# Optimization experiments

Hardware: AMD Instinct MI355X
Metric: run time of the kernel (lower is better)

The kernel has to match this reference:

```python
import jax, jax.numpy as jnp
import numpy as np

N = 13627        # n_nodes (from negative_sampling call in source)
E_EDGES = 504378 # n_edges
F_IN = 64
H1, H2, LIN_H = 300, 100, 100  # CONFIG HIDDEN_1/HIDDEN_2/LINEAR_HIDDEN


def setup_inputs() -> dict:
    key = jax.random.key(0)
    ks = jax.random.split(key, 10)
    x = jax.random.normal(ks[0], (N, F_IN), jnp.float32)
    edge_index = jax.random.randint(ks[1], (2, E_EDGES), 0, N, dtype=jnp.int64)
    neg_edge_index = jax.random.randint(ks[2], (2, E_EDGES), 0, N, dtype=jnp.int64)
    def w(k, shape):
        return jax.random.normal(k, shape, jnp.float32) * 0.05
    return dict(
        x=x, edge_index=edge_index, neg_edge_index=neg_edge_index,
        W1=w(ks[3], (2, F_IN, H1)), b1=jnp.zeros((H1,), jnp.float32),
        W2=w(ks[4], (2, H1, H2)), b2=jnp.zeros((H2,), jnp.float32),
        W3=w(ks[5], (2, H2, 1)), b3=jnp.zeros((1,), jnp.float32),
        linW1=w(ks[6], (F_IN, LIN_H)), linb1=jnp.zeros((LIN_H,), jnp.float32),
        linW2=w(ks[7], (F_IN, LIN_H)), linb2=jnp.zeros((LIN_H,), jnp.float32),
        c1=jnp.array([0.5], jnp.float32), c2=jnp.array([0.5], jnp.float32),
    )


def _cheb_norm(edge_index, n):
    # PyG ChebConv sym normalization with lambda_max=2: Lhat = L - I,
    # off-diagonal entries -deg[src]^-1/2 * deg[dst]^-1/2, diagonal 0.
    src, dst = edge_index[0], edge_index[1]
    deg = jax.ops.segment_sum(jnp.ones(src.shape, jnp.float32), src, num_segments=n)
    dinv = jnp.where(deg > 0, jax.lax.rsqrt(jnp.maximum(deg, 1.0)), 0.0)
    return -dinv[src] * dinv[dst]


def _cheb_conv(x, W, b, src, dst, norm, n):
    # K=2: out = Tx0 @ W[0] + Tx1 @ W[1] + b, with Tx1 = Lhat @ x (gather-scale-scatter)
    tx1 = jax.ops.segment_sum(norm[:, None] * x[src], dst, num_segments=n)
    return x @ W[0] + tx1 @ W[1] + b


def reference(x, edge_index, neg_edge_index, W1, b1, W2, b2, W3, b3,
              linW1, linb1, linW2, linb2, c1, c2):
    n = x.shape[0]
    src, dst = edge_index[0], edge_index[1]
    norm = _cheb_norm(edge_index, n)
    h = jax.nn.relu(_cheb_conv(x, W1, b1, src, dst, norm, n))
    x1 = jax.nn.relu(_cheb_conv(h, W2, b2, src, dst, norm, n))
    xo = x1 + jax.nn.relu(x @ linW1 + linb1)
    z = x1 + jax.nn.relu(x @ linW2 + linb2)
    pos = jax.nn.sigmoid(jnp.sum(z[edge_index[0]] * z[edge_index[1]], axis=1))
    pos_loss = -jnp.mean(jnp.log(pos + 1e-15))
    neg = jax.nn.sigmoid(jnp.sum(z[neg_edge_index[0]] * z[neg_edge_index[1]], axis=1))
    neg_loss = -jnp.mean(jnp.log(1.0 - neg + 1e-15))
    r_loss = pos_loss + neg_loss
    out = _cheb_conv(xo, W3, b3, src, dst, norm, n)
    return out, r_loss, c1, c2
```

## Files before the change

kernel.cpp:

```cpp
#include <hip/hip_runtime.h>
#include <math.h>


typedef unsigned short ushort_t;
typedef float v2f __attribute__((ext_vector_type(2)));
typedef short bf16x8 __attribute__((ext_vector_type(8)));
typedef float f32x4 __attribute__((ext_vector_type(4)));

#define GBM 64
#define GBN 64
#define GBK 32
#define LDK 72
#define HB  256
#define PACKN 6816

__device__ inline short f2bf(float f) {
    unsigned u = __float_as_uint(f);
    u += 0x7fff + ((u >> 16) & 1);
    return (short)(u >> 16);
}
__device__ inline float bflo(unsigned w) { return __uint_as_float(w << 16); }
__device__ inline float bfhi(unsigned w) { return __uint_as_float(w & 0xffff0000u); }

__device__ inline float dot16fp8(uint4 ra, uint4 rb) {
    float dot = 0.0f;
    v2f fa, fb;
    fa = __builtin_amdgcn_cvt_pk_f32_fp8(ra.x, false);
    fb = __builtin_amdgcn_cvt_pk_f32_fp8(rb.x, false);
    dot += fa.x * fb.x + fa.y * fb.y;
    fa = __builtin_amdgcn_cvt_pk_f32_fp8(ra.x, true);
    fb = __builtin_amdgcn_cvt_pk_f32_fp8(rb.x, true);
    dot += fa.x * fb.x + fa.y * fb.y;
    fa = __builtin_amdgcn_cvt_pk_f32_fp8(ra.y, false);
    fb = __builtin_amdgcn_cvt_pk_f32_fp8(rb.y, false);
    dot += fa.x * fb.x + fa.y * fb.y;
    fa = __builtin_amdgcn_cvt_pk_f32_fp8(ra.y, true);
    fb = __builtin_amdgcn_cvt_pk_f32_fp8(rb.y, true);
    dot += fa.x * fb.x + fa.y * fb.y;
    fa = __builtin_amdgcn_cvt_pk_f32_fp8(ra.z, false);
    fb = __builtin_amdgcn_cvt_pk_f32_fp8(rb.z, false);
    dot += fa.x * fb.x + fa.y * fb.y;
    fa = __builtin_amdgcn_cvt_pk_f32_fp8(ra.z, true);
    fb = __builtin_amdgcn_cvt_pk_f32_fp8(rb.z, true);
    dot += fa.x * fb.x + fa.y * fb.y;
    fa = __builtin_amdgcn_cvt_pk_f32_fp8(ra.w, false);
    fb = __builtin_amdgcn_cvt_pk_f32_fp8(rb.w, false);
    dot += fa.x * fb.x + fa.y * fb.y;
    fa = __builtin_amdgcn_cvt_pk_f32_fp8(ra.w, true);
    fb = __builtin_amdgcn_cvt_pk_f32_fp8(rb.w, true);
    dot += fa.x * fb.x + fa.y * fb.y;
    return dot;
}

__device__ inline float loss_term(float d, int y) {
    float sg = __builtin_amdgcn_rcpf(1.0f + __expf(-d));
    return y ? __logf(1.0f - sg + 1e-15f) : __logf(sg + 1e-15f);
}

__global__ __launch_bounds__(512) void hist_both_x_kernel(
    const int* __restrict__ ei, const float* __restrict__ x,
    int* __restrict__ degp, int* __restrict__ cntp,
    ushort_t* __restrict__ xb, int Nn, int E) {
    __shared__ int lhs[PACKN];
    __shared__ int lhd[PACKN];
    for (int i = threadIdx.x; i < PACKN; i += 512) { lhs[i] = 0; lhd[i] = 0; }
    __syncthreads();
    const int b = blockIdx.x;
    const int chunk = (E + HB - 1) / HB;
    const int e0 = b * chunk;
    const int e1 = (e0 + chunk < E) ? (e0 + chunk) : E;
    for (int e = e0 + threadIdx.x; e < e1; e += 512) {
        int s = ei[e], d = ei[E + e];
        atomicAdd(&lhs[s >> 1], 1 << ((s & 1) << 4));
        atomicAdd(&lhd[d >> 1], 1 << ((d & 1) << 4));
    }
    __syncthreads();
    int* ds = degp + (size_t)b * PACKN;
    int* cs = cntp + (size_t)b * PACKN;
    for (int i = threadIdx.x; i < PACKN; i += 512) { ds[i] = lhs[i]; cs[i] = lhd[i]; }
    const int rpb = (Nn + HB - 1) / HB;
    const int r0 = b * rpb;
    const int r1 = (r0 + rpb < Nn) ? (r0 + rpb) : Nn;
    for (int i = r0 * 64 + (int)threadIdx.x; i < r1 * 64; i += 512)
        xb[i] = (ushort_t)f2bf(x[i]);
}

__global__ void merge_kernel(const int* __restrict__ degp, const int* __restrict__ cntp,
                             ushort_t* __restrict__ off, int Nal,
                             float* __restrict__ dinv, int* __restrict__ rowptr,
                             float* __restrict__ acc, int n) {
    int tid = blockIdx.x * blockDim.x + threadIdx.x;
    if (tid == 0) {
        rowptr[0] = 0;
        acc[0] = 0.0f; acc[1] = 0.0f; acc[2] = 0.0f; acc[3] = 0.0f;
    }
    int v = tid >> 2, qq = tid & 3;
    if (v >= n) return;
    const int vh = v >> 1, sh = (v & 1) << 4;
    const int b0 = qq * (HB / 4), b1 = b0 + HB / 4;
    int dsum = 0, csum = 0;
    for (int b = b0; b < b1; ++b) {
        dsum += (degp[(size_t)b * PACKN + vh] >> sh) & 0xffff;
        csum += (cntp[(size_t)b * PACKN + vh] >> sh) & 0xffff;
    }
    int dtot = dsum;
    dtot += __shfl_xor(dtot, 1, 64);
    dtot += __shfl_xor(dtot, 2, 64);
    int inc = csum;
    int t = __shfl_up(inc, 1, 64); if (qq >= 1) inc += t;
    t = __shfl_up(inc, 2, 64);     if (qq >= 2) inc += t;
    int ex = inc - csum;
    if (qq == 0) dinv[v] = (dtot > 0) ? (1.0f / sqrtf((float)dtot)) : 0.0f;
    if (qq == 3) rowptr[v + 1] = inc;
    int run = ex;
    for (int b = b0; b < b1; ++b) {
        off[(size_t)b * Nal + v] = (ushort_t)run;
        run += (cntp[(size_t)b * PACKN + vh] >> sh) & 0xffff;
    }
}

__global__ void scan_kernel(int* __restrict__ rowptr, int n) {
    __shared__ int wsum[16];
    __shared__ int carry_s;
    if (threadIdx.x == 0) carry_s = 0;
    __syncthreads();
    int nchunk = (n + 1023) / 1024;
    int wid = threadIdx.x >> 6, lane = threadIdx.x & 63;
    for (int c = 0; c < nchunk; ++c) {
        int i = c * 1024 + threadIdx.x;
        int v = (i < n) ? rowptr[i + 1] : 0;
        int s = v;
        for (int off = 1; off < 64; off <<= 1) {
            int t = __shfl_up(s, off, 64);
            if (lane >= off) s += t;
        }
        if (lane == 63) wsum[wid] = s;
        __syncthreads();
        if (wid == 0 && lane < 16) {
            int wsv = wsum[lane];
            for (int off = 1; off < 16; off <<= 1) {
                int t = __shfl_up(wsv, off, 64);
                if (lane >= off) wsv += t;
            }
            wsum[lane] = wsv;
        }
        __syncthreads();
        int base = carry_s + (wid > 0 ? wsum[wid - 1] : 0);
        int inc = base + s;
        if (i < n) rowptr[i + 1] = inc;
        __syncthreads();
        if (threadIdx.x == 1023) carry_s = inc;
        __syncthreads();
    }
}

__global__ __launch_bounds__(512) void fill_lds_kernel(
    const int* __restrict__ ei, const float* __restrict__ dinv,
    const int* __restrict__ rowptr, const ushort_t* __restrict__ off, int Nal,
    int* __restrict__ colidx, float* __restrict__ wnorm, int E) {
    __shared__ int lh[PACKN];
    for (int i = threadIdx.x; i < PACKN; i += 512) lh[i] = 0;
    __syncthreads();
    const int b = blockIdx.x;
    const int chunk = (E + HB - 1) / HB;
    const int e0 = b * chunk;
    const int e1 = (e0 + chunk < E) ? (e0 + chunk) : E;
    const ushort_t* boff = off + (size_t)b * Nal;
    for (int e = e0 + threadIdx.x; e < e1; e += 512) {
        int s = ei[e], d = ei[E + e];
        int sh = (d & 1) << 4;
        int old = atomicAdd(&lh[d >> 1], 1 << sh);
        int rank = (old >> sh) & 0xffff;
        int slot = rowptr[d] + (int)boff[d] + rank;
        colidx[slot] = s;
        wnorm[slot] = -dinv[s] * dinv[d];
    }
}

__global__ void xt_kernel(const ushort_t* __restrict__ xb, const int* __restrict__ rowptr,
                          const int* __restrict__ colidx, const float* __restrict__ wnorm,
                          ushort_t* __restrict__ XTb, int n) {
    int node = (blockIdx.x * blockDim.x + threadIdx.x) >> 6;
    if (node >= n) return;
    int lane = threadIdx.x & 63;
    int grp = lane >> 4;
    int l = lane & 15;
    int j0 = rowptr[node], j1 = rowptr[node + 1];
    float a0 = 0, a1 = 0, a2 = 0, a3 = 0;
    int j = j0 + grp;
    if (j < j1) {
        float w = wnorm[j];
        int c = colidx[j];
        uint2 r = ((const uint2*)(xb + (size_t)c * 64))[l];
        for (;;) {
            int jn = j + 4;
            bool more = jn < j1;
            float wn = 0.0f;
            uint2 rn = r;
            if (more) {
                int cn = colidx[jn];
                wn = wnorm[jn];
                rn = ((const uint2*)(xb + (size_t)cn * 64))[l];
            }
            a0 += w * bflo(r.x); a1 += w * bfhi(r.x);
            a2 += w * bflo(r.y); a3 += w * bfhi(r.y);
            if (!more) break;
            j = jn; w = wn; r = rn;
        }
    }
    a0 += __shfl_xor(a0, 16, 64); a0 += __shfl_xor(a0, 32, 64);
    a1 += __shfl_xor(a1, 16, 64); a1 += __shfl_xor(a1, 32, 64);
    a2 += __shfl_xor(a2, 16, 64); a2 += __shfl_xor(a2, 32, 64);
    a3 += __shfl_xor(a3, 16, 64); a3 += __shfl_xor(a3, 32, 64);
    if (grp == 0) {
        uint2 xv = ((const uint2*)(xb + (size_t)node * 64))[l];
        *(uint2*)&XTb[(size_t)node * 128 + l * 4] = xv;
        uint2 p;
        p.x = (unsigned)(unsigned short)f2bf(a0) | ((unsigned)(unsigned short)f2bf(a1) << 16);
        p.y = (unsigned)(unsigned short)f2bf(a2) | ((unsigned)(unsigned short)f2bf(a3) << 16);
        *(uint2*)&XTb[(size_t)node * 128 + 64 + l * 4] = p;
    }
}

__global__ __launch_bounds__(256) void gemm_mfma(
    const float* __restrict__ A, const ushort_t* __restrict__ Abf, int lda,
    const float* __restrict__ B0, const float* __restrict__ B1,
    const float* __restrict__ bias0, const float* __restrict__ bias1,
    float* __restrict__ C, int ldc, ushort_t* __restrict__ Cbf, int ldcbf,
    int cbf_mode, int Nrows, int K, int Ncols, int split, int relu) {
    __shared__ short As[GBM * LDK];
    __shared__ short Bs[GBN * LDK];
    const int bm = blockIdx.y * GBM, bn = blockIdx.x * GBN;
    const int tid = threadIdx.x;
    const int w = tid >> 6, l = tid & 63;
    const int wm = (w >> 1) * 32, wn = (w & 1) * 32;
    const int lr = l & 15;
    const int kg = l >> 4;
    const int arow = tid >> 2, aseg = tid & 3;
    const int bcol = tid & 63, bk2 = (tid >> 6) * 2;
    const int ldb0 = split, ldb1 = Ncols - split;

    const int arowg = bm + arow;
    const int bcolg = bn + bcol;
    const float* Bsrc = (bcolg < split) ? (B0 + bcolg)
                       : ((bcolg < Ncols) ? (B1 + (bcolg - split)) : nullptr);
    const int ldb = (bcolg < split) ? ldb0 : ldb1;

    f32x4 acc00 = {0,0,0,0}, acc01 = {0,0,0,0}, acc10 = {0,0,0,0}, acc11 = {0,0,0,0};

    for (int k0 = 0; k0 < K; k0 += GBK) {
        {
            int kk = k0 + aseg * 8;
            bf16x8 v;
            if (Abf) {
                if (arowg < Nrows && kk + 7 < K) {
                    v = *(const bf16x8*)&Abf[(size_t)arowg * lda + kk];
                } else {
#pragma unroll
                    for (int i = 0; i < 8; ++i)
                        v[i] = (arowg < Nrows && kk + i < K)
                             ? (short)Abf[(size_t)arowg * lda + kk + i] : (short)0;
                }
            } else if (arowg < Nrows && kk + 7 < K) {
                float4 f0 = *(const float4*)&A[(size_t)arowg * lda + kk];
                float4 f1 = *(const float4*)&A[(size_t)arowg * lda + kk + 4];
                v[0] = f2bf(f0.x); v[1] = f2bf(f0.y); v[2] = f2bf(f0.z); v[3] = f2bf(f0.w);
                v[4] = f2bf(f1.x); v[5] = f2bf(f1.y); v[6] = f2bf(f1.z); v[7] = f2bf(f1.w);
            } else {
#pragma unroll
                for (int i = 0; i < 8; ++i)
                    v[i] = (arowg < Nrows && kk + i < K)
                         ? f2bf(A[(size_t)arowg * lda + kk + i]) : (short)0;
            }
            *(bf16x8*)&As[arow * LDK + aseg * 8] = v;
        }
#pragma unroll
        for (int q = 0; q < 4; ++q) {
            int k = q * 8 + bk2;
            unsigned pw = 0u;
            if (Bsrc) {
                float f0 = (k0 + k < K) ? Bsrc[(size_t)(k0 + k) * ldb] : 0.0f;
                float f1 = (k0 + k + 1 < K) ? Bsrc[(size_t)(k0 + k + 1) * ldb] : 0.0f;
                pw = (unsigned)(unsigned short)f2bf(f0)
                   | ((unsigned)(unsigned short)f2bf(f1) << 16);
            }
            *(unsigned*)&Bs[bcol * LDK + k] = pw;
        }
        __syncthreads();
        bf16x8 a0 = *(const bf16x8*)&As[(wm + lr) * LDK + kg * 8];
        bf16x8 a1 = *(const bf16x8*)&As[(wm + 16 + lr) * LDK + kg * 8];
        bf16x8 b0 = *(const bf16x8*)&Bs[(wn + lr) * LDK + kg * 8];
        bf16x8 b1 = *(const bf16x8*)&Bs[(wn + 16 + lr) * LDK + kg * 8];
        acc00 = __builtin_amdgcn_mfma_f32_16x16x32_bf16(a0, b0, acc00, 0, 0, 0);
        acc01 = __builtin_amdgcn_mfma_f32_16x16x32_bf16(a0, b1, acc01, 0, 0, 0);
        acc10 = __builtin_amdgcn_mfma_f32_16x16x32_bf16(a1, b0, acc10, 0, 0, 0);
        acc11 = __builtin_amdgcn_mfma_f32_16x16x32_bf16(a1, b1, acc11, 0, 0, 0);
        __syncthreads();
    }
#pragma unroll
    for (int i = 0; i < 2; ++i) {
        int rbase = bm + wm + i * 16 + kg * 4;
#pragma unroll
        for (int j = 0; j < 2; ++j) {
            int col = bn + wn + j * 16 + lr;
            if (col >= Ncols) continue;
            float bv = (col < split) ? (bias0 ? bias0[col] : 0.0f)
                                     : (bias1 ? bias1[col - split] : 0.0f);
            f32x4 a = (i == 0) ? (j == 0 ? acc00 : acc01) : (j == 0 ? acc10 : acc11);
#pragma unroll
            for (int r = 0; r < 4; ++r) {
                int row = rbase + r;
                if (row >= Nrows) continue;
                float o = a[r] + bv;
                if (relu) o = fmaxf(o, 0.0f);
                if (cbf_mode == 2)
                    Cbf[(size_t)row * ldcbf + col] = (ushort_t)f2bf(o);
                else if (cbf_mode == 1 && col >= split)
                    Cbf[(size_t)row * 128 + (col - split)] = (ushort_t)f2bf(o);
                else
                    C[(size_t)row * ldc + col] = o;
            }
        }
    }
}

__global__ void segsum_combine1_kernel(const ushort_t* __restrict__ hb,
                                       const int* __restrict__ rowptr, const int* __restrict__ colidx,
                                       const float* __restrict__ wnorm,
                                       const float* __restrict__ G2a, const float* __restrict__ b2,
                                       float* __restrict__ x1, int n) {
    int node = (blockIdx.x * blockDim.x + threadIdx.x) >> 6;
    if (node >= n) return;
    int lane = threadIdx.x & 63;
    int grp = lane >> 4;
    int l = lane & 15;
    int j0 = rowptr[node], j1 = rowptr[node + 1];
    float acc[8] = {};
    int j = j0 + grp;
    if (j < j1) {
        float w = wnorm[j];
        int c = colidx[j];
        uint4 r = ((const uint4*)(hb + (size_t)c * 128))[l];
        for (;;) {
            int jn = j + 4;
            bool more = jn < j1;
            float wn = 0.0f;
            uint4 rn = r;
            if (more) {
                int cn = colidx[jn];
                wn = wnorm[jn];
                rn = ((const uint4*)(hb + (size_t)cn * 128))[l];
            }
            acc[0] += w * bflo(r.x); acc[1] += w * bfhi(r.x);
            acc[2] += w * bflo(r.y); acc[3] += w * bfhi(r.y);
            acc[4] += w * bflo(r.z); acc[5] += w * bfhi(r.z);
            acc[6] += w * bflo(r.w); acc[7] += w * bfhi(r.w);
            if (!more) break;
            j = jn; w = wn; r = rn;
        }
    }
#pragma unroll
    for (int k = 0; k < 8; ++k) {
        acc[k] += __shfl_xor(acc[k], 16, 64);
        acc[k] += __shfl_xor(acc[k], 32, 64);
    }
    if (grp == 0) {
        int f = l * 8;
        if (f < 100) {
            float4 g0 = *(const float4*)&G2a[(size_t)node * 100 + f];
            float4 bv0 = *(const float4*)&b2[f];
            float4 o0;
            o0.x = fmaxf(g0.x + acc[0] + bv0.x, 0.0f);
            o0.y = fmaxf(g0.y + acc[1] + bv0.y, 0.0f);
            o0.z = fmaxf(g0.z + acc[2] + bv0.z, 0.0f);
            o0.w = fmaxf(g0.w + acc[3] + bv0.w, 0.0f);
            *(float4*)&x1[(size_t)node * 100 + f] = o0;
            if (f + 8 <= 100) {
                float4 g1 = *(const float4*)&G2a[(size_t)node * 100 + f + 4];
                float4 bv1 = *(const float4*)&b2[f + 4];
                float4 o1;
                o1.x = fmaxf(g1.x + acc[4] + bv1.x, 0.0f);
                o1.y = fmaxf(g1.y + acc[5] + bv1.y, 0.0f);
                o1.z = fmaxf(g1.z + acc[6] + bv1.z, 0.0f);
                o1.w = fmaxf(g1.w + acc[7] + bv1.w, 0.0f);
                *(float4*)&x1[(size_t)node * 100 + f + 4] = o1;
            }
        }
    }
}

__global__ void combine2_kernel(const float* __restrict__ S, const float* __restrict__ x1,
                                const float* __restrict__ w3b,
                                float* __restrict__ xo, unsigned* __restrict__ zf,
                                float* __restrict__ sv, int n) {
    int idx = blockIdx.x * blockDim.x + threadIdx.x;
    if (idx >= n * 32) return;
    int i = idx >> 5, q = idx & 31;
    unsigned w = 0u;
    float part = 0.0f;
    if (q < 25) {
        float4 s1 = *(const float4*)&S[(size_t)i * 200 + q * 4];
        float4 s2 = *(const float4*)&S[(size_t)i * 200 + 100 + q * 4];
        float4 xv = *(const float4*)&x1[(size_t)i * 100 + q * 4];
        float4 a, b;
        a.x = xv.x + fmaxf(s1.x, 0.0f); a.y = xv.y + fmaxf(s1.y, 0.0f);
        a.z = xv.z + fmaxf(s1.z, 0.0f); a.w = xv.w + fmaxf(s1.w, 0.0f);
        b.x = xv.x + fmaxf(s2.x, 0.0f); b.y = xv.y + fmaxf(s2.y, 0.0f);
        b.z = xv.z + fmaxf(s2.z, 0.0f); b.w = xv.w + fmaxf(s2.w, 0.0f);
        *(float4*)&xo[(size_t)i * 100 + q * 4] = a;
        w = (unsigned)__builtin_amdgcn_cvt_pk_fp8_f32(b.x, b.y, 0, false);
        w = (unsigned)__builtin_amdgcn_cvt_pk_fp8_f32(b.z, b.w, (int)w, true);
        float4 wv = *(const float4*)&w3b[q * 4];
        part = a.x * wv.x + a.y * wv.y + a.z * wv.z + a.w * wv.w;
    }
    zf[(size_t)i * 32 + q] = w;
#pragma unroll
    for (int off = 16; off > 0; off >>= 1)
        part += __shfl_xor(part, off, 32);
    if (q == 0) sv[i] = part;
}

__global__ __launch_bounds__(256) void edge_loss_fp8_kernel(
    const unsigned* __restrict__ zf, const int* __restrict__ ei,
    const int* __restrict__ nei, int E, float* __restrict__ accv) {
    const int y = blockIdx.y;
    const int* __restrict__ lst = y ? nei : ei;
    const int l = threadIdx.x & 7;
    const int g = (blockIdx.x * blockDim.x + threadIdx.x) >> 3;
    const int ng = (gridDim.x * blockDim.x) >> 3;
    const int stride2 = 2 * ng;
    float s = 0.0f;
    const int gA = g, gB = g + ng;
    int niterA = (gA < E) ? ((E - 1 - gA) / stride2 + 1) : 0;
    int niterB = (gB < E) ? ((E - 1 - gB) / stride2 + 1) : 0;
    if (niterA > 0) {
        int eB0 = (gB < E) ? gB : (E - 1);
        int eA1 = (gA + stride2 < E) ? (gA + stride2) : (E - 1);
        int eB1 = (gB + stride2 < E) ? (gB + stride2) : (E - 1);
        int aA0 = lst[gA], bA0 = lst[E + gA];
        int aB0 = lst[eB0], bB0 = lst[E + eB0];
        int aA1 = lst[eA1], bA1 = lst[E + eA1];
        int aB1 = lst[eB1], bB1 = lst[E + eB1];
        uint4 raA = *(const uint4*)&zf[(size_t)aA0 * 32 + l * 4];
        uint4 rbA = *(const uint4*)&zf[(size_t)bA0 * 32 + l * 4];
        uint4 raB = *(const uint4*)&zf[(size_t)aB0 * 32 + l * 4];
        uint4 rbB = *(const uint4*)&zf[(size_t)bB0 * 32 + l * 4];
        for (int t = 0; t < niterA; ++t) {
            int eA2 = gA + (t + 2) * stride2; eA2 = (eA2 < E) ? eA2 : (E - 1);
            int eB2 = gB + (t + 2) * stride2; eB2 = (eB2 < E) ? eB2 : (E - 1);
            int aA2 = lst[eA2], bA2 = lst[E + eA2];
            int aB2 = lst[eB2], bB2 = lst[E + eB2];
            uint4 raA1 = *(const uint4*)&zf[(size_t)aA1 * 32 + l * 4];
            uint4 rbA1 = *(const uint4*)&zf[(size_t)bA1 * 32 + l * 4];
            uint4 raB1 = *(const uint4*)&zf[(size_t)aB1 * 32 + l * 4];
            uint4 rbB1 = *(const uint4*)&zf[(size_t)bB1 * 32 + l * 4];
            float dA = dot16fp8(raA, rbA);
            float dB = dot16fp8(raB, rbB);
            dA += __shfl_xor(dA, 1, 8); dB += __shfl_xor(dB, 1, 8);
            dA += __shfl_xor(dA, 2, 8); dB += __shfl_xor(dB, 2, 8);
            dA += __shfl_xor(dA, 4, 8); dB += __shfl_xor(dB, 4, 8);
            if (l == 0) {
                s += loss_term(dA, y);
                if (t < niterB) s += loss_term(dB, y);
            }
            aA1 = aA2; bA1 = bA2; aB1 = aB2; bB1 = bB2;
            raA = raA1; rbA = rbA1; raB = raB1; rbB = rbB1;
        }
    }
    __shared__ float red[256];
    red[threadIdx.x] = s;
    __syncthreads();
    for (int st = 128; st > 0; st >>= 1) {
        if (threadIdx.x < st) red[threadIdx.x] += red[threadIdx.x + st];
        __syncthreads();
    }
    if (threadIdx.x == 0) atomicAdd(&accv[y], red[0]);
}

__global__ void out_finalize_kernel(const float* __restrict__ xo, const float* __restrict__ W3,
                                    const float* __restrict__ b3, const int* __restrict__ rowptr,
                                    const int* __restrict__ colidx, const float* __restrict__ wnorm,
                                    const float* __restrict__ sv, const float* __restrict__ accv,
                                    const float* __restrict__ c1, const float* __restrict__ c2,
                                    float* __restrict__ out, int n, int E) {
    int i = blockIdx.x * blockDim.x + threadIdx.x;
    if (i == 0) {
        out[n]     = -(accv[0] + accv[1]) / (float)E;
        out[n + 1] = c1[0];
        out[n + 2] = c2[0];
    }
    if (i >= n) return;
    const float4* a = (const float4*)(xo + (size_t)i * 100);
    const float4* wv = (const float4*)W3;
    float acc = b3[0];
#pragma unroll
    for (int q = 0; q < 25; ++q) {
        float4 va = a[q], vw = wv[q];
        acc += va.x * vw.x + va.y * vw.y + va.z * vw.z + va.w * vw.w;
    }
    int j1 = rowptr[i + 1];
    for (int j = rowptr[i]; j < j1; ++j)
        acc += wnorm[j] * sv[colidx[j]];
    out[i] = acc;
}

extern "C" void kernel_launch(void* const* d_in, const int* in_sizes, int n_in,
                              void* d_out, int out_size, void* d_ws, size_t ws_size,
                              hipStream_t stream) {
    (void)n_in; (void)out_size; (void)ws_size;
    const float* x   = (const float*)d_in[0];
    const int*   ei  = (const int*)d_in[1];
    const int*   nei = (const int*)d_in[2];
    const float* W1  = (const float*)d_in[3];
    const float* b1  = (const float*)d_in[4];
    const float* W2  = (const float*)d_in[5];
    const float* b2  = (const float*)d_in[6];
    const float* W3  = (const float*)d_in[7];
    const float* b3  = (const float*)d_in[8];
    const float* lw1 = (const float*)d_in[9];
    const float* lb1 = (const float*)d_in[10];
    const float* lw2 = (const float*)d_in[11];
    const float* lb2 = (const float*)d_in[12];
    const float* c1  = (const float*)d_in[13];
    const float* c2  = (const float*)d_in[14];

    const int Nn = in_sizes[0] / 64;
    const int E  = in_sizes[1] / 2;

    const size_t Nal = ((size_t)Nn + 5) & ~(size_t)3;
    const size_t Eal = ((size_t)E + 3) & ~(size_t)3;
    const int LDH = 304;

    float* ws       = (float*)d_ws;
    float* acc      = ws;
    float* dinv     = acc + 4;
    int*   rowptr   = (int*)(dinv + Nal);
    int*   colidx   = rowptr + Nal;
    float* wnorm    = (float*)(colidx + Eal);
    int*   degp     = (int*)(wnorm + Eal);
    int*   cntp     = degp + (size_t)HB * PACKN;
    ushort_t* offus = (ushort_t*)(cntp + (size_t)HB * PACKN);
    ushort_t* xb    = offus + (size_t)HB * Nal;
    ushort_t* XTb   = xb + (size_t)Nn * 64;
    ushort_t* hb    = XTb + (size_t)Nn * 128;
    float* G2a      = (float*)(hb + (size_t)Nn * LDH);
    float* x1       = G2a + (size_t)Nn * 100;
    float* xo       = x1 + (size_t)Nn * 100;
    float* S        = xo + (size_t)Nn * 100;
    size_t zoff     = (size_t)(S + (size_t)Nn * 200 - ws);
    zoff = (zoff + 31) & ~(size_t)31;
    unsigned* zf    = (unsigned*)(ws + zoff);
    size_t hoff2    = zoff + (size_t)Nn * 32 + 63;
    hoff2 &= ~(size_t)63;
    ushort_t* hWb   = (ushort_t*)(ws + hoff2);
    float* sv       = ws + hoff2 + (size_t)Nn * 64;
    const int MB = (Nn + GBM - 1) / GBM;

    hist_both_x_kernel<<<HB, 512, 0, stream>>>(ei, x, degp, cntp, xb, Nn, E);
    merge_kernel<<<(4 * Nn + 255) / 256, 256, 0, stream>>>(degp, cntp, offus, (int)Nal,
                                                           dinv, rowptr, acc, Nn);
    scan_kernel<<<1, 1024, 0, stream>>>(rowptr, Nn);
    fill_lds_kernel<<<HB, 512, 0, stream>>>(ei, dinv, rowptr, offus, (int)Nal,
                                            colidx, wnorm, E);

    xt_kernel<<<(Nn + 3) / 4, 256, 0, stream>>>(xb, rowptr, colidx, wnorm, XTb, Nn);
    gemm_mfma<<<dim3(5, MB), 256, 0, stream>>>(
        nullptr, XTb, 128, W1, nullptr, b1, nullptr,
        nullptr, 0, hb, LDH, 2, Nn, 128, 300, 300, 1);

    gemm_mfma<<<dim3(4, MB), 256, 0, stream>>>(
        nullptr, hb, LDH, W2, W2 + 300 * 100, nullptr, nullptr,
        G2a, 100, hWb, 0, 1, Nn, 300, 200, 100, 0);
    segsum_combine1_kernel<<<(Nn + 3) / 4, 256, 0, stream>>>(hWb, rowptr, colidx, wnorm,
                                                             G2a, b2, x1, Nn);

    gemm_mfma<<<dim3(4, MB), 256, 0, stream>>>(
        nullptr, xb, 64, lw1, lw2, lb1, lb2,
        S, 200, nullptr, 0, 0, Nn, 64, 200, 100, 0);
    combine2_kernel<<<(Nn * 32 + 255) / 256, 256, 0, stream>>>(S, x1, W3 + 100,
                                                               xo, zf, sv, Nn);

    edge_loss_fp8_kernel<<<dim3(1024, 2), 256, 0, stream>>>(zf, ei, nei, E, acc);

    out_finalize_kernel<<<(Nn + 255) / 256, 256, 0, stream>>>(
        xo, W3, b3, rowptr, colidx, wnorm, sv, acc, c1, c2, (float*)d_out, Nn, E);
}
```

Before: 215.7 us.

## Fuse linear-branch GEMMs into first ChebConv GEMM and restructure edge-loss loop

The first MFMA GEMM now computes three column groups at once (W1 over the full 128-wide [x, Lx] input plus lin1 and lin2 over only the first 64 K columns), which removes a separate GEMM launch and a second read of x. A new output mode writes the ReLU'd bf16 hidden activations and the fp32 linear outputs to separate buffers. The edge-loss kernel drops its software-pipelined prefetch in favour of processing four independent edges per iteration, and its grid is doubled. The fused GEMM wastes some K iterations on zero-padded B for the linear columns, and the edge kernel loses cross-iteration prefetch.

```diff
diff --git a/kernel.cpp b/kernel.cpp
--- a/kernel.cpp
+++ b/kernel.cpp
@@ -223,11 +223,12 @@
 }
 
 __global__ __launch_bounds__(256) void gemm_mfma(
-    const float* __restrict__ A, const ushort_t* __restrict__ Abf, int lda,
-    const float* __restrict__ B0, const float* __restrict__ B1,
-    const float* __restrict__ bias0, const float* __restrict__ bias1,
+    const ushort_t* __restrict__ Abf, int lda,
+    const float* __restrict__ B0, const float* __restrict__ B1, const float* __restrict__ B2,
+    const float* __restrict__ bias0, const float* __restrict__ bias1, const float* __restrict__ bias2,
+    int split, int split2, int klim1,
     float* __restrict__ C, int ldc, ushort_t* __restrict__ Cbf, int ldcbf,
-    int cbf_mode, int Nrows, int K, int Ncols, int split, int relu) {
+    int cbf_mode, int Nrows, int K, int Ncols, int relu) {
     __shared__ short As[GBM * LDK];
     __shared__ short Bs[GBN * LDK];
     const int bm = blockIdx.y * GBM, bn = blockIdx.x * GBN;
@@ -238,13 +239,14 @@
     const int kg = l >> 4;
     const int arow = tid >> 2, aseg = tid & 3;
     const int bcol = tid & 63, bk2 = (tid >> 6) * 2;
-    const int ldb0 = split, ldb1 = Ncols - split;
 
     const int arowg = bm + arow;
     const int bcolg = bn + bcol;
-    const float* Bsrc = (bcolg < split) ? (B0 + bcolg)
-                       : ((bcolg < Ncols) ? (B1 + (bcolg - split)) : nullptr);
-    const int ldb = (bcolg < split) ? ldb0 : ldb1;
+    const float* Bsrc = nullptr;
+    int ldb = 1, Klim = K;
+    if (bcolg < split)                            { Bsrc = B0 + bcolg; ldb = split; Klim = K; }
+    else if (bcolg < split2 && bcolg < Ncols)     { Bsrc = B1 + (bcolg - split); ldb = split2 - split; Klim = klim1; }
+    else if (bcolg < Ncols)                       { Bsrc = B2 + (bcolg - split2); ldb = Ncols - split2; Klim = klim1; }
 
     f32x4 acc00 = {0,0,0,0}, acc01 = {0,0,0,0}, acc10 = {0,0,0,0}, acc11 = {0,0,0,0};
 
@@ -252,25 +254,13 @@
         {
             int kk = k0 + aseg * 8;
             bf16x8 v;
-            if (Abf) {
-                if (arowg < Nrows && kk + 7 < K) {
-                    v = *(const bf16x8*)&Abf[(size_t)arowg * lda + kk];
-                } else {
-#pragma unroll
-                    for (int i = 0; i < 8; ++i)
-                        v[i] = (arowg < Nrows && kk + i < K)
-                             ? (short)Abf[(size_t)arowg * lda + kk + i] : (short)0;
-                }
-            } else if (arowg < Nrows && kk + 7 < K) {
-                float4 f0 = *(const float4*)&A[(size_t)arowg * lda + kk];
-                float4 f1 = *(const float4*)&A[(size_t)arowg * lda + kk + 4];
-                v[0] = f2bf(f0.x); v[1] = f2bf(f0.y); v[2] = f2bf(f0.z); v[3] = f2bf(f0.w);
-                v[4] = f2bf(f1.x); v[5] = f2bf(f1.y); v[6] = f2bf(f1.z); v[7] = f2bf(f1.w);
+            if (arowg < Nrows && kk + 7 < K) {
+                v = *(const bf16x8*)&Abf[(size_t)arowg * lda + kk];
             } else {
 #pragma unroll
                 for (int i = 0; i < 8; ++i)
                     v[i] = (arowg < Nrows && kk + i < K)
-                         ? f2bf(A[(size_t)arowg * lda + kk + i]) : (short)0;
+                         ? (short)Abf[(size_t)arowg * lda + kk + i] : (short)0;
             }
             *(bf16x8*)&As[arow * LDK + aseg * 8] = v;
         }
@@ -279,8 +269,8 @@
             int k = q * 8 + bk2;
             unsigned pw = 0u;
             if (Bsrc) {
-                float f0 = (k0 + k < K) ? Bsrc[(size_t)(k0 + k) * ldb] : 0.0f;
-                float f1 = (k0 + k + 1 < K) ? Bsrc[(size_t)(k0 + k + 1) * ldb] : 0.0f;
+                float f0 = (k0 + k < Klim) ? Bsrc[(size_t)(k0 + k) * ldb] : 0.0f;
+                float f1 = (k0 + k + 1 < Klim) ? Bsrc[(size_t)(k0 + k + 1) * ldb] : 0.0f;
                 pw = (unsigned)(unsigned short)f2bf(f0)
                    | ((unsigned)(unsigned short)f2bf(f1) << 16);
             }
@@ -304,21 +294,30 @@
         for (int j = 0; j < 2; ++j) {
             int col = bn + wn + j * 16 + lr;
             if (col >= Ncols) continue;
-            float bv = (col < split) ? (bias0 ? bias0[col] : 0.0f)
-                                     : (bias1 ? bias1[col - split] : 0.0f);
+            float bv;
+            if (col < split)       bv = bias0 ? bias0[col] : 0.0f;
+            else if (col < split2) bv = bias1 ? bias1[col - split] : 0.0f;
+            else                   bv = bias2 ? bias2[col - split2] : 0.0f;
             f32x4 a = (i == 0) ? (j == 0 ? acc00 : acc01) : (j == 0 ? acc10 : acc11);
 #pragma unroll
             for (int r = 0; r < 4; ++r) {
                 int row = rbase + r;
                 if (row >= Nrows) continue;
                 float o = a[r] + bv;
-                if (relu) o = fmaxf(o, 0.0f);
-                if (cbf_mode == 2)
+                if (cbf_mode == 3) {
+                    if (col < split)
+                        Cbf[(size_t)row * ldcbf + col] = (ushort_t)f2bf(fmaxf(o, 0.0f));
+                    else
+                        C[(size_t)row * ldc + (col - split)] = o;
+                } else if (cbf_mode == 2) {
+                    if (relu) o = fmaxf(o, 0.0f);
                     Cbf[(size_t)row * ldcbf + col] = (ushort_t)f2bf(o);
-                else if (cbf_mode == 1 && col >= split)
+                } else if (cbf_mode == 1 && col >= split) {
                     Cbf[(size_t)row * 128 + (col - split)] = (ushort_t)f2bf(o);
-                else
+                } else {
+                    if (relu) o = fmaxf(o, 0.0f);
                     C[(size_t)row * ldc + col] = o;
+                }
             }
         }
     }
@@ -428,43 +427,39 @@
     const int l = threadIdx.x & 7;
     const int g = (blockIdx.x * blockDim.x + threadIdx.x) >> 3;
     const int ng = (gridDim.x * blockDim.x) >> 3;
-    const int stride2 = 2 * ng;
+    const int stride4 = 4 * ng;
     float s = 0.0f;
-    const int gA = g, gB = g + ng;
-    int niterA = (gA < E) ? ((E - 1 - gA) / stride2 + 1) : 0;
-    int niterB = (gB < E) ? ((E - 1 - gB) / stride2 + 1) : 0;
-    if (niterA > 0) {
-        int eB0 = (gB < E) ? gB : (E - 1);
-        int eA1 = (gA + stride2 < E) ? (gA + stride2) : (E - 1);
-        int eB1 = (gB + stride2 < E) ? (gB + stride2) : (E - 1);
-        int aA0 = lst[gA], bA0 = lst[E + gA];
-        int aB0 = lst[eB0], bB0 = lst[E + eB0];
-        int aA1 = lst[eA1], bA1 = lst[E + eA1];
-        int aB1 = lst[eB1], bB1 = lst[E + eB1];
-        uint4 raA = *(const uint4*)&zf[(size_t)aA0 * 32 + l * 4];
-        uint4 rbA = *(const uint4*)&zf[(size_t)bA0 * 32 + l * 4];
-        uint4 raB = *(const uint4*)&zf[(size_t)aB0 * 32 + l * 4];
-        uint4 rbB = *(const uint4*)&zf[(size_t)bB0 * 32 + l * 4];
-        for (int t = 0; t < niterA; ++t) {
-            int eA2 = gA + (t + 2) * stride2; eA2 = (eA2 < E) ? eA2 : (E - 1);
-            int eB2 = gB + (t + 2) * stride2; eB2 = (eB2 < E) ? eB2 : (E - 1);
-            int aA2 = lst[eA2], bA2 = lst[E + eA2];
-            int aB2 = lst[eB2], bB2 = lst[E + eB2];
-            uint4 raA1 = *(const uint4*)&zf[(size_t)aA1 * 32 + l * 4];
-            uint4 rbA1 = *(const uint4*)&zf[(size_t)bA1 * 32 + l * 4];
-            uint4 raB1 = *(const uint4*)&zf[(size_t)aB1 * 32 + l * 4];
-            uint4 rbB1 = *(const uint4*)&zf[(size_t)bB1 * 32 + l * 4];
-            float dA = dot16fp8(raA, rbA);
-            float dB = dot16fp8(raB, rbB);
-            dA += __shfl_xor(dA, 1, 8); dB += __shfl_xor(dB, 1, 8);
-            dA += __shfl_xor(dA, 2, 8); dB += __shfl_xor(dB, 2, 8);
-            dA += __shfl_xor(dA, 4, 8); dB += __shfl_xor(dB, 4, 8);
-            if (l == 0) {
-                s += loss_term(dA, y);
-                if (t < niterB) s += loss_term(dB, y);
-            }
-            aA1 = aA2; bA1 = bA2; aB1 = aB2; bB1 = bB2;
-            raA = raA1; rbA = rbA1; raB = raB1; rbB = rbB1;
+    int n0 = (g < E) ? ((E - 1 - g) / stride4 + 1) : 0;
+    for (int t = 0; t < n0; ++t) {
+        int e[4]; bool valid[4];
+#pragma unroll
+        for (int k = 0; k < 4; ++k) {
+            int ee = g + k * ng + t * stride4;
+            valid[k] = (ee < E);
+            e[k] = valid[k] ? ee : (E - 1);
+        }
+        int ai[4], bi[4];
+#pragma unroll
+        for (int k = 0; k < 4; ++k) { ai[k] = lst[e[k]]; bi[k] = lst[E + e[k]]; }
+        uint4 ra[4], rb[4];
+#pragma unroll
+        for (int k = 0; k < 4; ++k) {
+            ra[k] = *(const uint4*)&zf[(size_t)ai[k] * 32 + l * 4];
+            rb[k] = *(const uint4*)&zf[(size_t)bi[k] * 32 + l * 4];
+        }
+        float d[4];
+#pragma unroll
+        for (int k = 0; k < 4; ++k) d[k] = dot16fp8(ra[k], rb[k]);
+#pragma unroll
+        for (int k = 0; k < 4; ++k) {
+            d[k] += __shfl_xor(d[k], 1, 8);
+            d[k] += __shfl_xor(d[k], 2, 8);
+            d[k] += __shfl_xor(d[k], 4, 8);
+        }
+        if (l == 0) {
+#pragma unroll
+            for (int k = 0; k < 4; ++k)
+                if (valid[k]) s += loss_term(d[k], y);
         }
     }
     __shared__ float red[256];
@@ -564,23 +559,20 @@
                                             colidx, wnorm, E);
 
     xt_kernel<<<(Nn + 3) / 4, 256, 0, stream>>>(xb, rowptr, colidx, wnorm, XTb, Nn);
-    gemm_mfma<<<dim3(5, MB), 256, 0, stream>>>(
-        nullptr, XTb, 128, W1, nullptr, b1, nullptr,
-        nullptr, 0, hb, LDH, 2, Nn, 128, 300, 300, 1);
+    gemm_mfma<<<dim3(8, MB), 256, 0, stream>>>(
+        XTb, 128, W1, lw1, lw2, b1, lb1, lb2,
+        300, 400, 64, S, 200, hb, LDH, 3, Nn, 128, 500, 1);
 
     gemm_mfma<<<dim3(4, MB), 256, 0, stream>>>(
-        nullptr, hb, LDH, W2, W2 + 300 * 100, nullptr, nullptr,
-        G2a, 100, hWb, 0, 1, Nn, 300, 200, 100, 0);
+        hb, LDH, W2, W2 + 300 * 100, W2 + 300 * 100, nullptr, nullptr, nullptr,
+        100, 200, 300, G2a, 100, hWb, 0, 1, Nn, 300, 200, 0);
     segsum_combine1_kernel<<<(Nn + 3) / 4, 256, 0, stream>>>(hWb, rowptr, colidx, wnorm,
                                                              G2a, b2, x1, Nn);
 
-    gemm_mfma<<<dim3(4, MB), 256, 0, stream>>>(
-        nullptr, xb, 64, lw1, lw2, lb1, lb2,
-        S, 200, nullptr, 0, 0, Nn, 64, 200, 100, 0);
     combine2_kernel<<<(Nn * 32 + 255) / 256, 256, 0, stream>>>(S, x1, W3 + 100,
                                                                xo, zf, sv, Nn);
 
-    edge_loss_fp8_kernel<<<dim3(1024, 2), 256, 0, stream>>>(zf, ei, nei, E, acc);
+    edge_loss_fp8_kernel<<<dim3(2048, 2), 256, 0, stream>>>(zf, ei, nei, E, acc);
 
     out_finalize_kernel<<<(Nn + 255) / 256, 256, 0, stream>>>(
         xo, W3, b3, rowptr, colidx, wnorm, sv, acc, c1, c2, (float*)d_out, Nn, E);
```

New measurement: 230.7 us. 7.0% more time.
